# Kernel tuning notes

Hardware: AMD Instinct MI355X
Metric: run time of the kernel (lower is better)

## Reference

```python
import jax, jax.numpy as jnp
import numpy as np

MU = 0.99
THRESHOLD = 1.0

def setup_inputs() -> dict:
    key = jax.random.key(0)
    k1, k2, k3 = jax.random.split(key, 3)
    N, W, T, K = 16, 512, 1024, 2048
    x = jax.random.normal(k1, (N, W, T), jnp.float32)
    k = jax.random.normal(k2, (K, W), jnp.float32) * 0.02
    k_sum = jax.random.normal(k3, (K, W), jnp.float32) * 0.02
    k_elem = jnp.ones((K,), jnp.float32)
    return {"x": x, "k": k, "k_sum": k_sum, "k_elem": k_elem}

def reference(x, k, k_sum, k_elem):
    N, W, T = x.shape
    K = k.shape[0]
    # preprocess: [N, W, T] -> [N*T, W]
    xf = x.transpose(0, 2, 1).reshape(-1, W)
    prenorm = jnp.linalg.norm(xf - jnp.mean(xf)) / np.sqrt(xf.size)
    # quantise: pairwise squared distances [N*T, K] then argmin
    dist = (jnp.sum(xf * xf, axis=-1, keepdims=True)
            - 2.0 * (xf @ k.T)
            + jnp.sum(k * k, axis=-1)[None, :])
    min_dist = jnp.min(dist, axis=-1)
    x_l = jnp.argmin(dist, axis=-1)
    fit = jnp.mean(min_dist)
    # dequantise: embedding gather
    x_d = k[x_l]
    # update_k: scatter-sum cluster stats + EMA + conditional reset (no grad)
    _k_sum = jax.ops.segment_sum(xf, x_l, num_segments=K)
    _k_elem = jax.ops.segment_sum(jnp.ones((xf.shape[0],), xf.dtype), x_l, num_segments=K)
    k_rand = jax.random.permutation(jax.random.key(42), xf)[:K]  # N*T >= K so no tiling
    k_sum_new = MU * k_sum + (1.0 - MU) * _k_sum
    k_elem_new = MU * k_elem + (1.0 - MU) * _k_elem
    usage = (k_elem_new[:, None] >= THRESHOLD).astype(xf.dtype)
    k_new = usage * (k_sum_new / k_elem_new[:, None]) + (1.0 - usage) * k_rand
    k_prob = _k_elem / jnp.sum(_k_elem)
    entropy = -jnp.sum(k_prob * jnp.log(k_prob + 1e-8))
    dk = jnp.linalg.norm(k_new - k) / np.sqrt(K * W)
    # commit loss + straight-through estimator
    commit_loss = jnp.sum((jax.lax.stop_gradient(x_d) - xf) ** 2) / xf.size
    x_d = xf + jax.lax.stop_gradient(x_d - xf)
    # postprocess
    x_d = x_d.reshape(N, T, W).transpose(0, 2, 1)
    x_l = x_l.reshape(N, T)
    return (x_l, x_d, commit_loss, fit, prenorm, entropy, dk, k_new, k_sum_new, k_elem_new)
```

## Files before the change

kernel.cpp:

```cpp
#include <hip/hip_runtime.h>
#include <stdint.h>
#include <algorithm>


#define W_   512
#define T_   1024
#define K_   2048
#define NT_  16384

#define XG_CAP 1536

typedef unsigned short ushort_t;
typedef __attribute__((ext_vector_type(8))) short short8;
typedef __attribute__((ext_vector_type(4))) float f32x4;

#define OFF_XHI     0u
#define OFF_XLO     16777216u
#define OFF_KHI     33554432u
#define OFF_KLO     35651584u
#define OFF_PM1     37748736u
#define OFF_PM2     39845888u
#define OFF_XG      37748736u
#define OFF_PACKED  40894464u
#define OFF_FLIST   41025536u
#define OFF_X2      41091072u
#define OFF_K2      41156608u
#define OFF_SCAL    41164800u
#define OFF_COUNTS  41165056u
#define OFF_CURSOR  41173248u
#define ZERO_LEN    16640u
#define OFF_OFFS    41443584u
#define OFF_ROWL    41452032u
#define OFF_KRAND   41517568u

#define O_XL    0u
#define O_XD    16384u
#define O_SC    8404992u
#define O_KNEW  8404997u
#define O_KSN   9453573u
#define O_KEN   10502149u

__device__ __forceinline__ float bf2f(ushort_t u) {
  return __uint_as_float(((unsigned)u) << 16);
}
__device__ __forceinline__ ushort_t f2bf(float v) {
  unsigned u = __float_as_uint(v);
  unsigned r = u + 0x7FFFu + ((u >> 16) & 1u);
  return (ushort_t)(r >> 16);
}
__device__ __forceinline__ void gload_lds16(const void* g, void* l) {
  __builtin_amdgcn_global_load_lds(
      (const __attribute__((address_space(1))) unsigned*)g,
      (__attribute__((address_space(3))) unsigned*)l, 16, 0, 0);
}

static inline void tf2x32_host(uint32_t k0, uint32_t k1, uint32_t x0, uint32_t x1,
                               uint32_t& o0, uint32_t& o1) {
  const uint32_t ks2 = k0 ^ k1 ^ 0x1BD11BDAu;
  x0 += k0; x1 += k1;
#define ROUND4(a,b,c,d) \
  x0+=x1; x1=(x1<<(a))|(x1>>(32-(a))); x1^=x0; \
  x0+=x1; x1=(x1<<(b))|(x1>>(32-(b))); x1^=x0; \
  x0+=x1; x1=(x1<<(c))|(x1>>(32-(c))); x1^=x0; \
  x0+=x1; x1=(x1<<(d))|(x1>>(32-(d))); x1^=x0;
  ROUND4(13,15,26,6)  x0+=k1;  x1+=ks2+1u;
  ROUND4(17,29,16,24) x0+=ks2; x1+=k0+2u;
  ROUND4(13,15,26,6)  x0+=k0;  x1+=k1+3u;
  ROUND4(17,29,16,24) x0+=k1;  x1+=ks2+4u;
  ROUND4(13,15,26,6)  x0+=ks2; x1+=k0+5u;
#undef ROUND4
  o0 = x0; o1 = x1;
}

static int h_krand[K_];
static bool h_krand_ready = false;

static void compute_krand_host() {
  static uint32_t bits1[NT_], bits2[NT_];
  static uint16_t rank1[NT_], rank2[NT_];
  static int idx[NT_];
  uint32_t a0, a1, b0, b1, c0, c1, d0, d1, o0, o1;
  tf2x32_host(0u, 42u, 0u, 0u, a0, a1);
  tf2x32_host(0u, 42u, 0u, 1u, b0, b1);
  tf2x32_host(a0, a1, 0u, 0u, c0, c1);
  tf2x32_host(a0, a1, 0u, 1u, d0, d1);
  (void)c0; (void)c1;
  for (uint32_t i = 0; i < NT_; i++) {
    tf2x32_host(b0, b1, 0u, i, o0, o1); bits1[i] = o1;
    tf2x32_host(d0, d1, 0u, i, o0, o1); bits2[i] = o1;
  }
  for (int i = 0; i < NT_; i++) idx[i] = i;
  std::stable_sort(idx, idx + NT_, [&](int a, int b) { return bits1[a] < bits1[b]; });
  for (int pos = 0; pos < NT_; pos++) rank1[idx[pos]] = (uint16_t)pos;
  for (int i = 0; i < NT_; i++) idx[i] = i;
  std::stable_sort(idx, idx + NT_, [&](int a, int b) { return bits2[a] < bits2[b]; });
  for (int pos = 0; pos < NT_; pos++) rank2[idx[pos]] = (uint16_t)pos;
  for (int i = 0; i < NT_; i++) {
    int j = rank1[i] & 16383;
    int p = rank2[j];
    if (p < K_) h_krand[p] = i;
  }
}

__global__ void vq_prep(const float* __restrict__ x, const float* __restrict__ k,
                        ushort_t* __restrict__ xhi, ushort_t* __restrict__ xlo,
                        float* __restrict__ x2, float* __restrict__ scal,
                        ushort_t* __restrict__ khi, ushort_t* __restrict__ klo,
                        float* __restrict__ k2v) {
  __shared__ float tile[64][65];
  __shared__ float x2s[64];
  __shared__ float rs[4], rq[4];
  int tid = threadIdx.x;
  if (blockIdx.x >= 256) {
    int row = (blockIdx.x - 256) * 8 + (tid >> 5);
    int wl = tid & 31;
    const float* kr = k + (size_t)row * 512;
    float acc = 0.f;
#pragma unroll
    for (int c = 0; c < 4; c++) {
      int w = c * 128 + wl * 4;
      float4 v = *(const float4*)(kr + w);
      ushort4 hv, lv;
      hv.x = f2bf(v.x); lv.x = f2bf(v.x - bf2f(hv.x));
      hv.y = f2bf(v.y); lv.y = f2bf(v.y - bf2f(hv.y));
      hv.z = f2bf(v.z); lv.z = f2bf(v.z - bf2f(hv.z));
      hv.w = f2bf(v.w); lv.w = f2bf(v.w - bf2f(hv.w));
      *(ushort4*)&khi[(size_t)row * 512 + w] = hv;
      *(ushort4*)&klo[(size_t)row * 512 + w] = lv;
      acc += v.x * v.x + v.y * v.y + v.z * v.z + v.w * v.w;
    }
    for (int off = 16; off; off >>= 1) acc += __shfl_down(acc, off, 32);
    if (wl == 0) k2v[row] = acc;
    return;
  }
  int b = blockIdx.x;
  int n = b >> 4, tc = b & 15;
  int t0 = tc * 64;
  if (tid < 64) x2s[tid] = 0.f;
  __syncthreads();
  float gs = 0.f, gq = 0.f;
  const size_t xb = (size_t)n * (W_ * T_);
  int tl = tid & 63, wg = tid >> 6;
  int wl = 2 * (tid & 31), tg = tid >> 5;
  for (int p = 0; p < 8; p++) {
    int w0 = p * 64;
#pragma unroll 4
    for (int s = 0; s < 16; s++) {
      int w = s * 4 + wg;
      tile[tl][w] = x[xb + (size_t)(w0 + w) * T_ + t0 + tl];
    }
    __syncthreads();
#pragma unroll
    for (int s = 0; s < 8; s++) {
      int t = s * 8 + tg;
      float v0 = tile[t][wl], v1 = tile[t][wl + 1];
      ushort_t h0 = f2bf(v0); ushort_t l0 = f2bf(v0 - bf2f(h0));
      ushort_t h1 = f2bf(v1); ushort_t l1 = f2bf(v1 - bf2f(h1));
      size_t row = (size_t)n * 1024 + t0 + t;
      ushort2 hv; hv.x = h0; hv.y = h1;
      ushort2 lv; lv.x = l0; lv.y = l1;
      *(ushort2*)&xhi[row * 512 + w0 + wl] = hv;
      *(ushort2*)&xlo[row * 512 + w0 + wl] = lv;
      gs += v0 + v1;
      float part = v0 * v0 + v1 * v1;
      gq += part;
      for (int off = 16; off; off >>= 1) part += __shfl_down(part, off, 32);
      if ((tid & 31) == 0) x2s[t] += part;
    }
    __syncthreads();
  }
  for (int off = 32; off; off >>= 1) { gs += __shfl_down(gs, off, 64); gq += __shfl_down(gq, off, 64); }
  if ((tid & 63) == 0) { rs[tid >> 6] = gs; rq[tid >> 6] = gq; }
  __syncthreads();
  if (tid == 0) {
    atomicAdd(&scal[0], rs[0] + rs[1] + rs[2] + rs[3]);
    atomicAdd(&scal[1], rq[0] + rq[1] + rq[2] + rq[3]);
  }
  if (tid < 64) x2[n * 1024 + t0 + tid] = x2s[tid];
}

__global__ __launch_bounds__(256, 2) void vq_argmin_mfma(
    const ushort_t* __restrict__ xhi, const ushort_t* __restrict__ xlo,
    const ushort_t* __restrict__ khi, const ushort_t* __restrict__ klo,
    const float* __restrict__ x2, const float* __restrict__ k2,
    unsigned long long* __restrict__ pm1, float* __restrict__ pm2) {
  __shared__ __align__(16) char smem[65536];
  int tid = threadIdx.x;
  int bx = blockIdx.x & 127, by = blockIdx.x >> 7;
  int row0 = bx * 128, col0 = by * 128;
  int lane = tid & 63, wid = tid >> 6;
  int wm = wid >> 1, wn = wid & 1;
  int lr = lane & 15, quad = lane >> 4;

  const char* gb[4];
  gb[0] = (const char*)xhi + (size_t)row0 * 1024;
  gb[1] = (const char*)xlo + (size_t)row0 * 1024;
  gb[2] = (const char*)khi + (size_t)col0 * 1024;
  gb[3] = (const char*)klo + (size_t)col0 * 1024;
  uint32_t goff[4], loff[4];
#pragma unroll
  for (int it = 0; it < 4; it++) {
    int cid = it * 256 + tid;
    int row = cid >> 3;
    int cc = (cid & 7) ^ (row & 7);
    goff[it] = row * 1024 + cc * 16;
    loff[it] = cid * 16;
  }
  uint32_t aoff[4], boff[4];
#pragma unroll
  for (int i = 0; i < 4; i++) {
    int ra = wm * 64 + i * 16 + lr;
    aoff[i] = ra * 128 + ((quad ^ (ra & 7)) * 16);
    int rb = wn * 64 + i * 16 + lr;
    boff[i] = rb * 128 + ((quad ^ (rb & 7)) * 16);
  }
  f32x4 acc[4][4] = {};

  for (int kt = 0; kt < 8; kt++) {
    uint32_t kofs = (uint32_t)kt * 128;
#pragma unroll
    for (int tl = 0; tl < 4; tl++)
#pragma unroll
      for (int it = 0; it < 4; it++)
        gload_lds16(gb[tl] + goff[it] + kofs, &smem[tl * 16384 + loff[it]]);
    __syncthreads();
#pragma unroll
    for (int kk = 0; kk < 2; kk++) {
      uint32_t kx = (uint32_t)kk << 6;
      short8 ah[4], al[4], bh[4], bl[4];
#pragma unroll
      for (int i = 0; i < 4; i++) {
        ah[i] = *(const short8*)&smem[(aoff[i] ^ kx)];
        al[i] = *(const short8*)&smem[16384 + (aoff[i] ^ kx)];
        bh[i] = *(const short8*)&smem[32768 + (boff[i] ^ kx)];
        bl[i] = *(const short8*)&smem[49152 + (boff[i] ^ kx)];
      }
#pragma unroll
      for (int i = 0; i < 4; i++)
#pragma unroll
        for (int j = 0; j < 4; j++) {
          acc[i][j] = __builtin_amdgcn_mfma_f32_16x16x32_bf16(ah[i], bh[j], acc[i][j], 0, 0, 0);
          acc[i][j] = __builtin_amdgcn_mfma_f32_16x16x32_bf16(ah[i], bl[j], acc[i][j], 0, 0, 0);
          acc[i][j] = __builtin_amdgcn_mfma_f32_16x16x32_bf16(al[i], bh[j], acc[i][j], 0, 0, 0);
        }
    }
    __syncthreads();
  }

  unsigned long long* L1 = (unsigned long long*)smem;
  float* L2f = (float*)&smem[33792];
  float k2c[4];
#pragma unroll
  for (int j = 0; j < 4; j++) k2c[j] = k2[col0 + wn * 64 + j * 16 + lr];
#pragma unroll
  for (int i = 0; i < 4; i++) {
#pragma unroll
    for (int r = 0; r < 4; r++) {
      int row_l = wm * 64 + i * 16 + quad * 4 + r;
      float x2r = x2[row0 + row_l];
      float m1 = 3.4e38f, m2 = 3.4e38f; int mi = 0;
#pragma unroll
      for (int j = 0; j < 4; j++) {
        float d = (x2r - 2.0f * acc[i][j][r]) + k2c[j];
        int kg = col0 + wn * 64 + j * 16 + lr;
        if (d < m1) { m2 = m1; m1 = d; mi = kg; } else m2 = fminf(m2, d);
      }
      L1[row_l * 33 + wn * 16 + lr] =
          (((unsigned long long)__float_as_uint(m1)) << 32) | (unsigned)mi;
      L2f[row_l * 33 + wn * 16 + lr] = m2;
    }
  }
  __syncthreads();
  if (tid < 128) {
    unsigned long long b1 = L1[tid * 33];
    float b2 = L2f[tid * 33];
    for (int c = 1; c < 32; c++) {
      unsigned long long v = L1[tid * 33 + c];
      float vf = L2f[tid * 33 + c];
      if (v < b1) { b2 = fminf(b2, __uint_as_float((unsigned)(b1 >> 32))); b1 = v; }
      else b2 = fminf(b2, __uint_as_float((unsigned)(v >> 32)));
      b2 = fminf(b2, vf);
    }
    pm1[(size_t)by * NT_ + row0 + tid] = b1;
    pm2[(size_t)by * NT_ + row0 + tid] = b2;
  }
}

__global__ void vq_merge(const unsigned long long* __restrict__ pm1,
                         const float* __restrict__ pm2,
                         unsigned long long* __restrict__ packed,
                         int* __restrict__ flist, int* __restrict__ nflag) {
  int r = blockIdx.x * 256 + threadIdx.x;
  unsigned long long b1 = pm1[r];
  float b2 = pm2[r];
  for (int c = 1; c < 16; c++) {
    unsigned long long v = pm1[(size_t)c * NT_ + r];
    float vf = pm2[(size_t)c * NT_ + r];
    if (v < b1) { b2 = fminf(b2, __uint_as_float((unsigned)(b1 >> 32))); b1 = v; }
    else b2 = fminf(b2, __uint_as_float((unsigned)(v >> 32)));
    b2 = fminf(b2, vf);
  }
  if ((b2 - __uint_as_float((unsigned)(b1 >> 32))) < 3e-4f) {
    packed[r] = 0xFFFFFFFFFFFFFFFFull;
    int pos = atomicAdd(nflag, 1);
    flist[pos] = r;
  } else {
    packed[r] = b1;
  }
}

__global__ void vq_gatherx(const float* __restrict__ x, const int* __restrict__ flist,
                           const int* __restrict__ nflag, float* __restrict__ xg) {
  int nf = *nflag; if (nf > XG_CAP) nf = XG_CAP;
  int total = nf * 512;
  for (int e = blockIdx.x * 256 + threadIdx.x; e < total; e += gridDim.x * 256) {
    int ii = e >> 9, c = e & 511;
    int r = flist[ii];
    xg[e] = x[(size_t)(r >> 10) * 524288 + (size_t)c * 1024 + (r & 1023)];
  }
}

__global__ void vq_repair(const float* __restrict__ x, const float* __restrict__ k,
                          const float* __restrict__ xg,
                          const float* __restrict__ x2, const float* __restrict__ k2,
                          const int* __restrict__ flist, const int* __restrict__ nflag,
                          unsigned long long* __restrict__ packed) {
  __shared__ float xs[8][512];
  __shared__ unsigned long long part[8][4];
  int tid = threadIdx.x;
  int lane = tid & 63, wave = tid >> 6;
  int nf = *nflag;
  int ngrp = (nf + 7) >> 3;
  int nwork = ngrp * 8;
  for (int wi = blockIdx.x; wi < nwork; wi += gridDim.x) {
    int g = wi >> 3, c = wi & 7;
    int base = g * 8;
    for (int e = tid; e < 8 * 512; e += 256) {
      int rr = e >> 9, cc = e & 511;
      int ii = base + rr;
      float v = 0.f;
      if (ii < nf) {
        if (ii < XG_CAP) v = xg[ii * 512 + cc];
        else { int r = flist[ii]; v = x[(size_t)(r >> 10) * 524288 + (size_t)cc * 1024 + (r & 1023)]; }
      }
      xs[rr][cc] = v;
    }
    __syncthreads();
    int j = c * 256 + tid;
    const float4* kr = (const float4*)(k + (size_t)j * 512);
    float dot[8] = {0.f, 0.f, 0.f, 0.f, 0.f, 0.f, 0.f, 0.f};
    for (int w4 = 0; w4 < 128; w4++) {
      float4 kv = kr[w4];
#pragma unroll
      for (int rr = 0; rr < 8; rr++) {
        const float4 xv = *(const float4*)&xs[rr][w4 * 4];
        dot[rr] = fmaf(xv.x, kv.x, dot[rr]);
        dot[rr] = fmaf(xv.y, kv.y, dot[rr]);
        dot[rr] = fmaf(xv.z, kv.z, dot[rr]);
        dot[rr] = fmaf(xv.w, kv.w, dot[rr]);
      }
    }
    float k2j = k2[j];
#pragma unroll
    for (int rr = 0; rr < 8; rr++) {
      int ii = base + rr;
      unsigned long long pv = 0xFFFFFFFFFFFFFFFFull;
      if (ii < nf) {
        int r = flist[ii];
        float d = (x2[r] - 2.0f * dot[rr]) + k2j;
        pv = (((unsigned long long)__float_as_uint(d)) << 32) | (unsigned)j;
      }
      for (int off = 32; off; off >>= 1) {
        unsigned long long o = __shfl_down(pv, off, 64);
        if (o < pv) pv = o;
      }
      if (lane == 0) part[rr][wave] = pv;
    }
    __syncthreads();
    if (tid < 8) {
      int ii = base + tid;
      if (ii < nf) {
        unsigned long long m = part[tid][0];
        if (part[tid][1] < m) m = part[tid][1];
        if (part[tid][2] < m) m = part[tid][2];
        if (part[tid][3] < m) m = part[tid][3];
        atomicMin(&packed[flist[ii]], m);
      }
    }
    __syncthreads();
  }
}

__global__ void vq_cnt2(const unsigned long long* __restrict__ packed,
                        float* __restrict__ counts, float* __restrict__ scal,
                        float* __restrict__ out) {
  int tid = threadIdx.x;
  int r = blockIdx.x * 256 + tid;
  unsigned long long p = packed[r];
  unsigned idx = (unsigned)(p & 0xFFFFFFFFull);
  float md = __uint_as_float((unsigned)(p >> 32));
  out[O_XL + r] = (float)idx;
  atomicAdd(&counts[idx], 1.0f);
  float s = md;
  for (int off = 32; off; off >>= 1) s += __shfl_down(s, off, 64);
  __shared__ float rs[4];
  if ((tid & 63) == 0) rs[tid >> 6] = s;
  __syncthreads();
  if (tid == 0) atomicAdd(&scal[2], rs[0] + rs[1] + rs[2] + rs[3]);
}

__global__ void vq_scan(const float* __restrict__ counts, int* __restrict__ offs) {
  __shared__ int wsum[4];
  int t = threadIdx.x;
  int loc[8];
  int s = 0;
#pragma unroll
  for (int c = 0; c < 8; c++) { loc[c] = (int)counts[t * 8 + c]; s += loc[c]; }
  int orig = s;
  int lane = t & 63, wave = t >> 6;
#pragma unroll
  for (int off = 1; off < 64; off <<= 1) {
    int v = __shfl_up(s, off, 64);
    if (lane >= off) s += v;
  }
  if (lane == 63) wsum[wave] = s;
  __syncthreads();
  int add = 0;
  for (int w = 0; w < 4; w++) if (w < wave) add += wsum[w];
  int excl = s + add - orig;
#pragma unroll
  for (int c = 0; c < 8; c++) {
    offs[t * 8 + c] = excl;
    excl += loc[c];
  }
  if (t == 255) offs[2048] = excl;
}

__global__ void vq_fill_xd(const unsigned long long* __restrict__ packed,
                           const int* __restrict__ offs, int* __restrict__ cursor,
                           int* __restrict__ rowl, const float* __restrict__ k,
                           float* __restrict__ out) {
  __shared__ int lrow[64];
  int tid = threadIdx.x;
  if (blockIdx.x < 64) {
    int r = blockIdx.x * 256 + tid;
    int idx = (int)(packed[r] & 0xFFFFFFFFull);
    int pos = atomicAdd(&cursor[idx], 1);
    rowl[offs[idx] + pos] = r;
    return;
  }
  int bid = blockIdx.x - 64;
  int tb = bid >> 2, wq = bid & 3;
  int row0 = tb * 64;
  int n = row0 >> 10, t0 = row0 & 1023;
  if (tid < 64) lrow[tid] = (int)(packed[row0 + tid] & 0xFFFFFFFFull);
  __syncthreads();
  int tq = (tid & 15) * 4;
  int wl = tid >> 4;
  const float* k0 = k + (size_t)lrow[tq + 0] * 512;
  const float* k1 = k + (size_t)lrow[tq + 1] * 512;
  const float* k2r = k + (size_t)lrow[tq + 2] * 512;
  const float* k3 = k + (size_t)lrow[tq + 3] * 512;
  float* xd = out + O_XD + (size_t)n * 524288 + t0 + tq;
#pragma unroll
  for (int it = 0; it < 8; it++) {
    int w = wq * 128 + it * 16 + wl;
    float4 v;
    v.x = k0[w]; v.y = k1[w]; v.z = k2r[w]; v.w = k3[w];
    *(float4*)&xd[(size_t)w * 1024] = v;
  }
}

__global__ void vq_knew_csr(const ushort_t* __restrict__ xhi, const ushort_t* __restrict__ xlo,
                            const float* __restrict__ k, const float* __restrict__ ksum_in,
                            const float* __restrict__ kelem_in, const int* __restrict__ offs,
                            const int* __restrict__ rowl, const int* __restrict__ krand,
                            float* __restrict__ out, float* __restrict__ scal) {
  int j = blockIdx.x, tid = threadIdx.x;
  int o0 = offs[j], o1 = offs[j + 1];
  int w0 = tid * 2;
  float s0 = 0.f, s1 = 0.f;
  int p = o0;
  for (; p + 1 < o1; p += 2) {
    int ra = rowl[p], rb = rowl[p + 1];
    uint32_t ha = *(const uint32_t*)&xhi[(size_t)ra * 512 + w0];
    uint32_t la = *(const uint32_t*)&xlo[(size_t)ra * 512 + w0];
    uint32_t hb = *(const uint32_t*)&xhi[(size_t)rb * 512 + w0];
    uint32_t lb = *(const uint32_t*)&xlo[(size_t)rb * 512 + w0];
    s0 += bf2f((ushort_t)ha) + bf2f((ushort_t)la);
    s1 += bf2f((ushort_t)(ha >> 16)) + bf2f((ushort_t)(la >> 16));
    s0 += bf2f((ushort_t)hb) + bf2f((ushort_t)lb);
    s1 += bf2f((ushort_t)(hb >> 16)) + bf2f((ushort_t)(lb >> 16));
  }
  if (p < o1) {
    int ra = rowl[p];
    uint32_t ha = *(const uint32_t*)&xhi[(size_t)ra * 512 + w0];
    uint32_t la = *(const uint32_t*)&xlo[(size_t)ra * 512 + w0];
    s0 += bf2f((ushort_t)ha) + bf2f((ushort_t)la);
    s1 += bf2f((ushort_t)(ha >> 16)) + bf2f((ushort_t)(la >> 16));
  }
  float cnt = (float)(o1 - o0);
  float ken = 0.99f * kelem_in[j] + 0.01f * cnt;
  bool use = (ken >= 1.0f);
  int ir = krand[j] & 16383;
  float2 ks = *(const float2*)&ksum_in[(size_t)j * 512 + w0];
  float2 kc = *(const float2*)&k[(size_t)j * 512 + w0];
  float ksn0 = 0.99f * ks.x + 0.01f * s0;
  float ksn1 = 0.99f * ks.y + 0.01f * s1;
  out[O_KSN + (size_t)j * 512 + w0]     = ksn0;
  out[O_KSN + (size_t)j * 512 + w0 + 1] = ksn1;
  float kn0, kn1;
  if (use) {
    float inv = 1.0f / ken;
    kn0 = ksn0 * inv; kn1 = ksn1 * inv;
  } else {
    uint32_t hr = *(const uint32_t*)&xhi[(size_t)ir * 512 + w0];
    uint32_t lr = *(const uint32_t*)&xlo[(size_t)ir * 512 + w0];
    kn0 = bf2f((ushort_t)hr) + bf2f((ushort_t)lr);
    kn1 = bf2f((ushort_t)(hr >> 16)) + bf2f((ushort_t)(lr >> 16));
  }
  out[O_KNEW + (size_t)j * 512 + w0]     = kn0;
  out[O_KNEW + (size_t)j * 512 + w0 + 1] = kn1;
  float d0 = kn0 - kc.x, d1 = kn1 - kc.y;
  float dd = d0 * d0 + d1 * d1;
  for (int off = 32; off; off >>= 1) dd += __shfl_down(dd, off, 64);
  __shared__ float r4[4];
  if ((tid & 63) == 0) r4[tid >> 6] = dd;
  __syncthreads();
  if (tid == 0) {
    atomicAdd(&scal[3], r4[0] + r4[1] + r4[2] + r4[3]);
    out[O_KEN + j] = ken;
  }
}

__global__ void vq_fin(const float* __restrict__ counts, const float* __restrict__ scal,
                       float* __restrict__ out) {
  int tid = threadIdx.x;
  float e = 0.f;
  for (int j = tid; j < K_; j += 256) {
    float p = counts[j] * (1.0f / 16384.0f);
    e -= p * logf(p + 1e-8f);
  }
  for (int off = 32; off; off >>= 1) e += __shfl_down(e, off, 64);
  __shared__ float r[4];
  if ((tid & 63) == 0) r[tid >> 6] = e;
  __syncthreads();
  if (tid == 0) {
    float ent = r[0] + r[1] + r[2] + r[3];
    float sum = scal[0], sumsq = scal[1], fits = scal[2], d2 = scal[3];
    const float S = 8388608.f;
    out[O_SC + 0] = fits / S;
    out[O_SC + 1] = fits / 16384.f;
    out[O_SC + 2] = sqrtf((sumsq - sum * sum / S) / S);
    out[O_SC + 3] = ent;
    out[O_SC + 4] = sqrtf(d2 / 1048576.f);
  }
}

extern "C" void kernel_launch(void* const* d_in, const int* in_sizes, int n_in,
                              void* d_out, int out_size, void* d_ws, size_t ws_size,
                              hipStream_t stream) {
  (void)in_sizes; (void)n_in; (void)out_size; (void)ws_size;
  const float* x        = (const float*)d_in[0];
  const float* k        = (const float*)d_in[1];
  const float* ksum_in  = (const float*)d_in[2];
  const float* kelem_in = (const float*)d_in[3];
  float* out = (float*)d_out;
  uint8_t* ws = (uint8_t*)d_ws;

  ushort_t* xhi = (ushort_t*)(ws + OFF_XHI);
  ushort_t* xlo = (ushort_t*)(ws + OFF_XLO);
  ushort_t* khi = (ushort_t*)(ws + OFF_KHI);
  ushort_t* klo = (ushort_t*)(ws + OFF_KLO);
  unsigned long long* pm1 = (unsigned long long*)(ws + OFF_PM1);
  float*    pm2    = (float*)(ws + OFF_PM2);
  float*    xg     = (float*)(ws + OFF_XG);
  unsigned long long* packed = (unsigned long long*)(ws + OFF_PACKED);
  int*      flist  = (int*)(ws + OFF_FLIST);
  float*    x2v    = (float*)(ws + OFF_X2);
  float*    k2v    = (float*)(ws + OFF_K2);
  float*    scal   = (float*)(ws + OFF_SCAL);
  int*      nflag  = (int*)(ws + OFF_SCAL + 32);
  float*    counts = (float*)(ws + OFF_COUNTS);
  int*      cursor = (int*)(ws + OFF_CURSOR);
  int*      offs   = (int*)(ws + OFF_OFFS);
  int*      rowl   = (int*)(ws + OFF_ROWL);
  int*      krand  = (int*)(ws + OFF_KRAND);

  if (!h_krand_ready) { compute_krand_host(); h_krand_ready = true; }

  hipMemsetAsync(ws + OFF_SCAL, 0, ZERO_LEN, stream);
  hipMemcpyAsync(krand, h_krand, sizeof(h_krand), hipMemcpyHostToDevice, stream);

  vq_prep<<<512, 256, 0, stream>>>(x, k, xhi, xlo, x2v, scal, khi, klo, k2v);
  vq_argmin_mfma<<<2048, 256, 0, stream>>>(xhi, xlo, khi, klo, x2v, k2v, pm1, pm2);
  vq_merge<<<64, 256, 0, stream>>>(pm1, pm2, packed, flist, nflag);
  vq_gatherx<<<256, 256, 0, stream>>>(x, flist, nflag, xg);
  vq_repair<<<512, 256, 0, stream>>>(x, k, xg, x2v, k2v, flist, nflag, packed);
  vq_cnt2<<<64, 256, 0, stream>>>(packed, counts, scal, out);
  vq_scan<<<1, 256, 0, stream>>>(counts, offs);
  vq_fill_xd<<<1088, 256, 0, stream>>>(packed, offs, cursor, rowl, k, out);
  vq_knew_csr<<<2048, 256, 0, stream>>>(xhi, xlo, k, ksum_in, kelem_in, offs, rowl, krand, out, scal);
  vq_fin<<<1, 256, 0, stream>>>(counts, scal, out);
}
```

Before: 322.3 us.

## Double-buffer argmin GEMM K-slices with async LDS loads and vmcnt waits

Restructures the MFMA distance GEMM main loop into two half-K phases, each with its own 32KB LDS buffer. Global-to-LDS loads for the next K slice are issued right after the current fragments are read into registers, so memory traffic overlaps with MFMA work. Partial vmcnt waits replace full syncthreads, and the LDS swizzle is changed to match the 64-byte row stride. MFMA sections run at raised wave priority. This adds manual waitcnt and barrier ordering, which must be exactly right to avoid data races.

```diff
diff --git a/kernel.cpp b/kernel.cpp
--- a/kernel.cpp
+++ b/kernel.cpp
@@ -179,6 +179,46 @@
   if (tid < 64) x2[n * 1024 + t0 + tid] = x2s[tid];
 }
 
+template <int VM, bool DO_ISSUE>
+__device__ __forceinline__ void argmin_phase(
+    char* smem, const char* const gb[4], const uint32_t goff[2], const uint32_t loff[2],
+    const uint32_t aoff[4], const uint32_t boff[4], int ph, int ktn,
+    f32x4 (&acc)[4][4]) {
+  if (VM == 8) asm volatile("s_waitcnt vmcnt(8)" ::: "memory");
+  else         asm volatile("s_waitcnt vmcnt(0)" ::: "memory");
+  __builtin_amdgcn_s_barrier();
+  const char* base = smem + ph * 32768;
+  short8 ah[4], al[4], bh[4], bl[4];
+#pragma unroll
+  for (int i = 0; i < 4; i++) {
+    ah[i] = *(const short8*)(base +         aoff[i]);
+    al[i] = *(const short8*)(base +  8192 + aoff[i]);
+    bh[i] = *(const short8*)(base + 16384 + boff[i]);
+    bl[i] = *(const short8*)(base + 24576 + boff[i]);
+  }
+  asm volatile("s_waitcnt lgkmcnt(0)" ::: "memory");
+  __builtin_amdgcn_sched_barrier(0);
+  __builtin_amdgcn_s_barrier();
+  if (DO_ISSUE) {
+#pragma unroll
+    for (int arr = 0; arr < 4; arr++)
+#pragma unroll
+      for (int it = 0; it < 2; it++)
+        gload_lds16(gb[arr] + goff[it] + ph * 64 + ktn * 128,
+                    smem + ph * 32768 + arr * 8192 + loff[it]);
+  }
+  __builtin_amdgcn_s_setprio(1);
+#pragma unroll
+  for (int i = 0; i < 4; i++)
+#pragma unroll
+    for (int j = 0; j < 4; j++) {
+      acc[i][j] = __builtin_amdgcn_mfma_f32_16x16x32_bf16(ah[i], bh[j], acc[i][j], 0, 0, 0);
+      acc[i][j] = __builtin_amdgcn_mfma_f32_16x16x32_bf16(ah[i], bl[j], acc[i][j], 0, 0, 0);
+      acc[i][j] = __builtin_amdgcn_mfma_f32_16x16x32_bf16(al[i], bh[j], acc[i][j], 0, 0, 0);
+    }
+  __builtin_amdgcn_s_setprio(0);
+}
+
 __global__ __launch_bounds__(256, 2) void vq_argmin_mfma(
     const ushort_t* __restrict__ xhi, const ushort_t* __restrict__ xlo,
     const ushort_t* __restrict__ khi, const ushort_t* __restrict__ klo,
@@ -197,55 +237,41 @@
   gb[1] = (const char*)xlo + (size_t)row0 * 1024;
   gb[2] = (const char*)khi + (size_t)col0 * 1024;
   gb[3] = (const char*)klo + (size_t)col0 * 1024;
-  uint32_t goff[4], loff[4];
-#pragma unroll
-  for (int it = 0; it < 4; it++) {
+  uint32_t goff[2], loff[2];
+#pragma unroll
+  for (int it = 0; it < 2; it++) {
     int cid = it * 256 + tid;
-    int row = cid >> 3;
-    int cc = (cid & 7) ^ (row & 7);
+    int row = cid >> 2;
+    int swr = (row ^ (row >> 2)) & 3;
+    int cc = (cid & 3) ^ swr;
     goff[it] = row * 1024 + cc * 16;
     loff[it] = cid * 16;
   }
+  int swl = (lr ^ (lr >> 2)) & 3;
   uint32_t aoff[4], boff[4];
 #pragma unroll
   for (int i = 0; i < 4; i++) {
     int ra = wm * 64 + i * 16 + lr;
-    aoff[i] = ra * 128 + ((quad ^ (ra & 7)) * 16);
+    aoff[i] = ra * 64 + ((quad ^ swl) & 3) * 16;
     int rb = wn * 64 + i * 16 + lr;
-    boff[i] = rb * 128 + ((quad ^ (rb & 7)) * 16);
+    boff[i] = rb * 64 + ((quad ^ swl) & 3) * 16;
   }
   f32x4 acc[4][4] = {};
 
-  for (int kt = 0; kt < 8; kt++) {
-    uint32_t kofs = (uint32_t)kt * 128;
-#pragma unroll
-    for (int tl = 0; tl < 4; tl++)
-#pragma unroll
-      for (int it = 0; it < 4; it++)
-        gload_lds16(gb[tl] + goff[it] + kofs, &smem[tl * 16384 + loff[it]]);
-    __syncthreads();
-#pragma unroll
-    for (int kk = 0; kk < 2; kk++) {
-      uint32_t kx = (uint32_t)kk << 6;
-      short8 ah[4], al[4], bh[4], bl[4];
-#pragma unroll
-      for (int i = 0; i < 4; i++) {
-        ah[i] = *(const short8*)&smem[(aoff[i] ^ kx)];
-        al[i] = *(const short8*)&smem[16384 + (aoff[i] ^ kx)];
-        bh[i] = *(const short8*)&smem[32768 + (boff[i] ^ kx)];
-        bl[i] = *(const short8*)&smem[49152 + (boff[i] ^ kx)];
-      }
-#pragma unroll
-      for (int i = 0; i < 4; i++)
-#pragma unroll
-        for (int j = 0; j < 4; j++) {
-          acc[i][j] = __builtin_amdgcn_mfma_f32_16x16x32_bf16(ah[i], bh[j], acc[i][j], 0, 0, 0);
-          acc[i][j] = __builtin_amdgcn_mfma_f32_16x16x32_bf16(ah[i], bl[j], acc[i][j], 0, 0, 0);
-          acc[i][j] = __builtin_amdgcn_mfma_f32_16x16x32_bf16(al[i], bh[j], acc[i][j], 0, 0, 0);
-        }
-    }
-    __syncthreads();
-  }
+#pragma unroll
+  for (int ph = 0; ph < 2; ph++)
+#pragma unroll
+    for (int arr = 0; arr < 4; arr++)
+#pragma unroll
+      for (int it = 0; it < 2; it++)
+        gload_lds16(gb[arr] + goff[it] + ph * 64, smem + ph * 32768 + arr * 8192 + loff[it]);
+
+  for (int kt = 0; kt < 7; kt++) {
+    argmin_phase<8, true>(smem, gb, goff, loff, aoff, boff, 0, kt + 1, acc);
+    argmin_phase<8, true>(smem, gb, goff, loff, aoff, boff, 1, kt + 1, acc);
+  }
+  argmin_phase<8, false>(smem, gb, goff, loff, aoff, boff, 0, 0, acc);
+  argmin_phase<0, false>(smem, gb, goff, loff, aoff, boff, 1, 0, acc);
 
   unsigned long long* L1 = (unsigned long long*)smem;
   float* L2f = (float*)&smem[33792];
```

Result: slower. 329.5 us (+2.2%).
